# Performance work log

Measured on AMD Instinct MI355X. Metric: run time of the kernel, lower is better.

Reference implementation:

```python
import jax, jax.numpy as jnp
import numpy as np

N_NODES = 100000
N_EDGES = 1600000
IN_SIZE = 512
HID_SIZE = 256
OUT_SIZE = 16
DROP_P = 0.5


def _degrees(idx, n):
    d = jax.ops.segment_sum(jnp.ones(idx.shape[0], jnp.float32), idx, num_segments=n)
    return jnp.maximum(d, 1.0)  # DGL clamps zero degrees to 1


def graph_conv(src, dst, feat, W, b, activation=None):
    # DGL GraphConv, norm='both': D_in^{-1/2} A D_out^{-1/2} X W + b
    n = feat.shape[0]
    inv_sqrt_dout = _degrees(src, n) ** -0.5   # out-degree of source nodes
    inv_sqrt_din = _degrees(dst, n) ** -0.5    # in-degree of destination nodes
    h = feat * inv_sqrt_dout[:, None]
    h = h @ W  # in_feats >= out_feats -> transform before aggregation (same math)
    # message passing: scatter-add source messages to destinations
    h = jax.ops.segment_sum(h[src], dst, num_segments=n)
    h = h * inv_sqrt_din[:, None] + b
    if activation is not None:
        h = activation(h)
    return h


def setup_inputs() -> dict:
    key = jax.random.key(0)
    ks = jax.random.split(key, 9)
    features = jax.random.normal(ks[0], (N_NODES, IN_SIZE), jnp.float32)
    src = jax.random.randint(ks[1], (N_EDGES,), 0, N_NODES)
    dst = jax.random.randint(ks[2], (N_EDGES,), 0, N_NODES)
    W1 = jax.random.normal(ks[3], (IN_SIZE, HID_SIZE), jnp.float32) / np.sqrt(IN_SIZE).astype(np.float32)
    b1 = jnp.zeros((HID_SIZE,), jnp.float32)
    W2 = jax.random.normal(ks[4], (HID_SIZE, HID_SIZE), jnp.float32) / np.sqrt(HID_SIZE).astype(np.float32)
    b2 = jnp.zeros((HID_SIZE,), jnp.float32)
    W3 = jax.random.normal(ks[5], (HID_SIZE, OUT_SIZE), jnp.float32) / np.sqrt(HID_SIZE).astype(np.float32)
    b3 = jnp.zeros((OUT_SIZE,), jnp.float32)
    return {"features": features, "src": src, "dst": dst,
            "W1": W1, "b1": b1, "W2": W2, "b2": b2, "W3": W3, "b3": b3}


def reference(features, src, dst, W1, b1, W2, b2, W3, b3):
    # layer 0: GraphConv + relu
    h = graph_conv(src, dst, features, W1, b1, activation=jax.nn.relu)
    # dropout(0.5) before layer 1 (deterministic fixed-key mask, training semantics)
    keep = jax.random.bernoulli(jax.random.key(42), 1.0 - DROP_P, h.shape)
    h = jnp.where(keep, h / (1.0 - DROP_P), 0.0)
    # layer 1: GraphConv (no activation)
    h = graph_conv(src, dst, h, W2, b2, activation=None)
    # layer 2: plain Linear head
    return h @ W3 + b3
```

## Files before the change

### kernel.cpp

```cpp
#include <hip/hip_runtime.h>
#include <stdint.h>

#define NN    100000
#define NE    1600000
#define IN_F  512
#define HID   256
#define OUTF  16
#define NPAD  100096
#define NBK   391
#define EPB   8192

typedef unsigned int u32;
typedef __bf16 bfrag  __attribute__((ext_vector_type(8)));
typedef float  f32x4  __attribute__((ext_vector_type(4)));
typedef short  s16x8  __attribute__((ext_vector_type(8)));

__device__ __forceinline__ u32 rotl32(u32 x, int r){ return (x<<r)|(x>>(32-r)); }

__device__ __forceinline__ bool drop_keep(u32 i){
    const u32 ks0 = 0u, ks1 = 42u, ks2 = 0x1BD11BDAu ^ 0u ^ 42u;
    u32 x0 = 0u + ks0;
    u32 x1 = i  + ks1;
#define TFR(r) { x0 += x1; x1 = rotl32(x1,(r)); x1 ^= x0; }
    TFR(13) TFR(15) TFR(26) TFR(6)   x0 += ks1; x1 += ks2 + 1u;
    TFR(17) TFR(29) TFR(16) TFR(24)  x0 += ks2; x1 += ks0 + 2u;
    TFR(13) TFR(15) TFR(26) TFR(6)   x0 += ks0; x1 += ks1 + 3u;
    TFR(17) TFR(29) TFR(16) TFR(24)  x0 += ks1; x1 += ks2 + 4u;
    TFR(13) TFR(15) TFR(26) TFR(6)   x0 += ks2; x1 += ks0 + 5u;
#undef TFR
    return ((x0 ^ x1) >> 31) == 0u;
}

__device__ __forceinline__ short f2b(float f){
    union { float f; u32 u; } v; v.f = f;
    u32 r = (v.u + 0x7FFFu + ((v.u >> 16) & 1u)) >> 16;
    return (short)r;
}
__device__ __forceinline__ float blo(u32 u){ union{u32 u; float f;} v; v.u = u << 16;         return v.f; }
__device__ __forceinline__ float bhi(u32 u){ union{u32 u; float f;} v; v.u = u & 0xFFFF0000u; return v.f; }

__device__ __forceinline__ u32 cvt_pk_bf16(float lo, float hi){
    u32 r;
    asm("v_cvt_pk_bf16_f32 %0, %1, %2" : "=v"(r) : "v"(lo), "v"(hi));
    return r;
}

__device__ __forceinline__ void gll16(const void* g, void* l){
    __builtin_amdgcn_global_load_lds((const __attribute__((address_space(1))) void*)g,
                                     (__attribute__((address_space(3))) void*)l, 16, 0, 0);
}


__global__ __launch_bounds__(256) void build_hist(const int4* __restrict__ src4,
                                                  const int4* __restrict__ dst4,
                                                  int* deg_out, int* __restrict__ bcnt){
    __shared__ int h[NBK];
    int t = threadIdx.x;
    for (int i = t; i < NBK; i += 256) h[i] = 0;
    __syncthreads();
    for (int i = blockIdx.x * 256 + t; i < NE / 4; i += gridDim.x * 256) {
        int4 s = src4[i];
        int4 d = dst4[i];
        atomicAdd(&deg_out[s.x], 1);
        atomicAdd(&deg_out[s.y], 1);
        atomicAdd(&deg_out[s.z], 1);
        atomicAdd(&deg_out[s.w], 1);
        atomicAdd(&h[d.x >> 8], 1);
        atomicAdd(&h[d.y >> 8], 1);
        atomicAdd(&h[d.z >> 8], 1);
        atomicAdd(&h[d.w >> 8], 1);
    }
    __syncthreads();
    for (int i = t; i < NBK; i += 256)
        if (h[i]) atomicAdd(&bcnt[i], h[i]);
}

__global__ __launch_bounds__(256) void finalize_deg(const int* __restrict__ deg_out,
                                                    const int* __restrict__ row_ptr,
                                                    float* isdo, float* isdi){
    int i = blockIdx.x * blockDim.x + threadIdx.x;
    if (i < NN) {
        isdo[i] = rsqrtf(fmaxf((float)deg_out[i], 1.0f));
        isdi[i] = rsqrtf(fmaxf((float)(row_ptr[i + 1] - row_ptr[i]), 1.0f));
    }
}

__global__ __launch_bounds__(512) void bucket_scan(const int* __restrict__ bcnt,
                                                   int* __restrict__ bbase,
                                                   int* __restrict__ bcur,
                                                   int* __restrict__ row_ptr){
    __shared__ int sh[512];
    int t = threadIdx.x;
    int v = (t < NBK) ? bcnt[t] : 0;
    sh[t] = v;
    __syncthreads();
    for (int off = 1; off < 512; off <<= 1) {
        int a = (t >= off) ? sh[t - off] : 0;
        __syncthreads();
        sh[t] += a;
        __syncthreads();
    }
    int excl = sh[t] - v;
    if (t < NBK) { bbase[t] = excl; bcur[t] = excl; }
    if (t == 0)  { bbase[NBK] = NE; row_ptr[NN] = NE; }
}

__global__ __launch_bounds__(256) void bucket_scatter(const int* __restrict__ src,
                                                      const int* __restrict__ dst,
                                                      int* bcur, u32* __restrict__ tmp){
    __shared__ int lh[NBK];
    __shared__ int lb[NBK];
    int t = threadIdx.x;
    for (int i = t; i < NBK; i += 256) lh[i] = 0;
    __syncthreads();
    const int e0 = blockIdx.x * EPB;
    for (int k = t * 4; k < EPB; k += 1024) {
        int e = e0 + k;
        if (e < NE) {
            int4 d = *(const int4*)(dst + e);
            atomicAdd(&lh[d.x >> 8], 1);
            atomicAdd(&lh[d.y >> 8], 1);
            atomicAdd(&lh[d.z >> 8], 1);
            atomicAdd(&lh[d.w >> 8], 1);
        }
    }
    __syncthreads();
    for (int i = t; i < NBK; i += 256) {
        int c = lh[i];
        if (c) lb[i] = atomicAdd(&bcur[i], c);
        lh[i] = 0;
    }
    __syncthreads();
    for (int k = t * 4; k < EPB; k += 1024) {
        int e = e0 + k;
        if (e < NE) {
            int4 d = *(const int4*)(dst + e);
            int4 s = *(const int4*)(src + e);
            int b0 = d.x >> 8, b1 = d.y >> 8, b2 = d.z >> 8, b3 = d.w >> 8;
            int r0 = atomicAdd(&lh[b0], 1);
            tmp[lb[b0] + r0] = ((u32)s.x << 8) | ((u32)d.x & 255u);
            int r1 = atomicAdd(&lh[b1], 1);
            tmp[lb[b1] + r1] = ((u32)s.y << 8) | ((u32)d.y & 255u);
            int r2 = atomicAdd(&lh[b2], 1);
            tmp[lb[b2] + r2] = ((u32)s.z << 8) | ((u32)d.z & 255u);
            int r3 = atomicAdd(&lh[b3], 1);
            tmp[lb[b3] + r3] = ((u32)s.w << 8) | ((u32)d.w & 255u);
        }
    }
}

__global__ __launch_bounds__(256) void bucket_finalize(const u32* __restrict__ tmp,
                                                       const int* __restrict__ bbase,
                                                       int* __restrict__ row_ptr,
                                                       int* __restrict__ col_src){
    __shared__ int h[256];
    __shared__ int wtot[4];
    const int t = threadIdx.x;
    const int b = blockIdx.x;
    const int base = bbase[b];
    const int cnt  = bbase[b + 1] - base;
    h[t] = 0;
    __syncthreads();
    for (int k = t; k < cnt; k += 256)
        atomicAdd(&h[tmp[base + k] & 255u], 1);
    __syncthreads();
    int v = h[t];
    int lane = t & 63, w = t >> 6;
    int s = v;
    #pragma unroll
    for (int off = 1; off < 64; off <<= 1) {
        int u = __shfl_up(s, off);
        if (lane >= off) s += u;
    }
    if (lane == 63) wtot[w] = s;
    __syncthreads();
    int woff = 0;
    #pragma unroll
    for (int i = 0; i < 4; ++i) woff += (i < w) ? wtot[i] : 0;
    int excl = woff + s - v;
    int d = (b << 8) + t;
    if (d < NN) row_ptr[d] = base + excl;
    h[t] = excl;
    __syncthreads();
    for (int k = t; k < cnt; k += 256) {
        u32 p = tmp[base + k];
        int r = atomicAdd(&h[p & 255u], 1);
        col_src[base + r] = (int)(p >> 8);
    }
}


template<int Kd, int Nd>
__global__ __launch_bounds__(256) void convert_wt(const float* __restrict__ W,
                                                  short* __restrict__ WT){
    int i = blockIdx.x * 256 + threadIdx.x;
    if (i >= Kd * Nd) return;
    int n = i / Kd, k = i - n * Kd;
    WT[i] = f2b(W[(size_t)k * Nd + n]);
}

__global__ __launch_bounds__(256) void gemm_x(const float* __restrict__ X,
                                              const short* __restrict__ BT,
                                              const float* __restrict__ isdo,
                                              short* __restrict__ C){
    __shared__ __align__(16) float As[2 * 4096];
    __shared__ __align__(16) short Bs[2 * 4096];

    const int t = threadIdx.x;
    const int wave = t >> 6, lane = t & 63;
    const int bm = blockIdx.x * 128;
    const int bn = blockIdx.y * 128;

    const int gsw = lane ^ ((lane >> 3) & 7);
    const int rl  = gsw >> 1;
    const int pp  = gsw & 1;
    const float* pa0 = X + (size_t)(((bm + 0*32 + rl) < NN) ? (bm + 0*32 + rl) : 0) * IN_F + wave * 8 + pp * 4;
    const float* pa1 = X + (size_t)(((bm + 1*32 + rl) < NN) ? (bm + 1*32 + rl) : 0) * IN_F + wave * 8 + pp * 4;
    const float* pa2 = X + (size_t)(((bm + 2*32 + rl) < NN) ? (bm + 2*32 + rl) : 0) * IN_F + wave * 8 + pp * 4;
    const float* pa3 = X + (size_t)(((bm + 3*32 + rl) < NN) ? (bm + 3*32 + rl) : 0) * IN_F + wave * 8 + pp * 4;

    const int ch0 = wave * 128 + lane;
    const int ch1 = ch0 + 64;
    const int kb0 = ch0 >> 7, r0 = ch0 & 127;
    const int kb1 = ch1 >> 7, r1 = ch1 & 127;
    const short* pb0 = BT + (size_t)(bn + r0) * IN_F + kb0 * 8;
    const short* pb1 = BT + (size_t)(bn + r1) * IN_F + kb1 * 8;

    const int wr = (wave >> 1) * 64, wc = (wave & 1) * 64;
    const int kq = lane >> 4, r15 = lane & 15;

    f32x4 acc[4][4];
    #pragma unroll
    for (int m = 0; m < 4; ++m)
        #pragma unroll
        for (int n = 0; n < 4; ++n) acc[m][n] = (f32x4)0.0f;

#define STAGE_X(BUF, K0) { \
    float* lA = As + (BUF) * 4096 + wave * 1024; \
    gll16(pa0 + (K0), lA);       gll16(pa1 + (K0), lA + 256); \
    gll16(pa2 + (K0), lA + 512); gll16(pa3 + (K0), lA + 768); \
    short* lb = Bs + (BUF) * 4096 + (size_t)(wave * 128) * 8; \
    gll16(pb0 + (K0), lb);       gll16(pb1 + (K0), lb + 512); }

#define COMPUTE_X(BUF) { \
    const float* AsC = As + (BUF) * 4096; \
    const short* BsC = Bs + (BUF) * 4096; \
    const short* fbC = BsC + (size_t)(kq * 128 + wc + r15) * 8; \
    bfrag af[4], bfg[4]; \
    _Pragma("unroll") \
    for (int m = 0; m < 4; ++m) { \
        int r  = wr + m * 16 + r15; \
        int j  = r >> 5, rr = r & 31; \
        int g0 = 2 * rr;  int G0 = g0 ^ ((g0 >> 3) & 7); \
        int g1 = g0 + 1;  int G1 = g1 ^ ((g1 >> 3) & 7); \
        const float* base = AsC + kq * 1024 + j * 256; \
        float4 f0 = *(const float4*)(base + G0 * 4); \
        float4 f1 = *(const float4*)(base + G1 * 4); \
        uint4 q = make_uint4(cvt_pk_bf16(f0.x, f0.y), cvt_pk_bf16(f0.z, f0.w), \
                             cvt_pk_bf16(f1.x, f1.y), cvt_pk_bf16(f1.z, f1.w)); \
        af[m] = *(bfrag*)&q; \
    } \
    _Pragma("unroll") \
    for (int n = 0; n < 4; ++n) bfg[n] = *(const bfrag*)(fbC + n * 128); \
    _Pragma("unroll") \
    for (int m = 0; m < 4; ++m) \
        _Pragma("unroll") \
        for (int n = 0; n < 4; ++n) \
            acc[m][n] = __builtin_amdgcn_mfma_f32_16x16x32_bf16(af[m], bfg[n], acc[m][n], 0, 0, 0); }

    const int NT = IN_F / 32;
    STAGE_X(0, 0);
    int cur = 0;
    for (int tt = 0; tt < NT - 1; ++tt) {
        STAGE_X(cur ^ 1, (tt + 1) * 32);
        asm volatile("s_waitcnt vmcnt(6)" ::: "memory");
        __builtin_amdgcn_s_barrier();
        COMPUTE_X(cur);
        asm volatile("" ::: "memory");
        __builtin_amdgcn_s_barrier();
        cur ^= 1;
    }
    asm volatile("s_waitcnt vmcnt(0)" ::: "memory");
    __builtin_amdgcn_s_barrier();
    COMPUTE_X(cur);
#undef STAGE_X
#undef COMPUTE_X

    const int crow0 = bm + wr + (lane >> 4) * 4;
    const int ccol0 = bn + wc + (lane & 15);
    #pragma unroll
    for (int m = 0; m < 4; ++m)
        #pragma unroll
        for (int r = 0; r < 4; ++r) {
            int row = crow0 + m * 16 + r;
            float sc = (row < NN) ? isdo[row] : 0.0f;
            #pragma unroll
            for (int n = 0; n < 4; ++n)
                C[(size_t)row * HID + ccol0 + n * 16] = f2b(acc[m][n][r] * sc);
        }
}

template<int K>
__global__ __launch_bounds__(256) void gemm_bt(const short* __restrict__ A,
                                               const short* __restrict__ BT,
                                               short* __restrict__ C){
    __shared__ __align__(16) short As[2 * 4096];
    __shared__ __align__(16) short Bs[2 * 4096];

    const int t = threadIdx.x;
    const int wave = t >> 6, lane = t & 63;
    const int bm = blockIdx.x * 128;
    const int bn = blockIdx.y * 128;

    const int ch0 = wave * 128 + lane;
    const int ch1 = ch0 + 64;
    const int kb0 = ch0 >> 7, r0 = ch0 & 127;
    const int kb1 = ch1 >> 7, r1 = ch1 & 127;
    const short* pa0 = A  + (size_t)(bm + r0) * K + kb0 * 8;
    const short* pa1 = A  + (size_t)(bm + r1) * K + kb1 * 8;
    const short* pb0 = BT + (size_t)(bn + r0) * K + kb0 * 8;
    const short* pb1 = BT + (size_t)(bn + r1) * K + kb1 * 8;

    const int wr = (wave >> 1) * 64, wc = (wave & 1) * 64;
    const int frag_off = ((lane >> 4) * 128 + (lane & 15)) * 8;

    f32x4 acc[4][4];
    #pragma unroll
    for (int m = 0; m < 4; ++m)
        #pragma unroll
        for (int n = 0; n < 4; ++n) acc[m][n] = (f32x4)0.0f;

#define STAGE_B(BUF, K0) { \
    short* la = As + (BUF) * 4096 + (size_t)(wave * 128) * 8; \
    short* lb = Bs + (BUF) * 4096 + (size_t)(wave * 128) * 8; \
    gll16(pa0 + (K0), la); gll16(pa1 + (K0), la + 512); \
    gll16(pb0 + (K0), lb); gll16(pb1 + (K0), lb + 512); }

#define COMPUTE_B(BUF) { \
    const short* fa = As + (BUF) * 4096 + frag_off + wr * 8; \
    const short* fb = Bs + (BUF) * 4096 + frag_off + wc * 8; \
    bfrag af[4], bfg[4]; \
    _Pragma("unroll") \
    for (int m = 0; m < 4; ++m) af[m]  = *(const bfrag*)(fa + m * 128); \
    _Pragma("unroll") \
    for (int n = 0; n < 4; ++n) bfg[n] = *(const bfrag*)(fb + n * 128); \
    _Pragma("unroll") \
    for (int m = 0; m < 4; ++m) \
        _Pragma("unroll") \
        for (int n = 0; n < 4; ++n) \
            acc[m][n] = __builtin_amdgcn_mfma_f32_16x16x32_bf16(af[m], bfg[n], acc[m][n], 0, 0, 0); }

    const int NT = K / 32;
    STAGE_B(0, 0);
    int cur = 0;
    for (int tt = 0; tt < NT - 1; ++tt) {
        STAGE_B(cur ^ 1, (tt + 1) * 32);
        asm volatile("s_waitcnt vmcnt(4)" ::: "memory");
        __builtin_amdgcn_s_barrier();
        COMPUTE_B(cur);
        asm volatile("" ::: "memory");
        __builtin_amdgcn_s_barrier();
        cur ^= 1;
    }
    asm volatile("s_waitcnt vmcnt(0)" ::: "memory");
    __builtin_amdgcn_s_barrier();
    COMPUTE_B(cur);
#undef STAGE_B
#undef COMPUTE_B

    const int crow0 = bm + wr + (lane >> 4) * 4;
    const int ccol0 = bn + wc + (lane & 15);
    #pragma unroll
    for (int m = 0; m < 4; ++m)
        #pragma unroll
        for (int n = 0; n < 4; ++n)
            #pragma unroll
            for (int r = 0; r < 4; ++r)
                C[(size_t)(crow0 + m * 16 + r) * HID + ccol0 + n * 16] = f2b(acc[m][n][r]);
}

template<int MODE>
__global__ __launch_bounds__(256) void gather_agg(const short* __restrict__ H,
                                                  const int* __restrict__ rp,
                                                  const int* __restrict__ cs,
                                                  const float* __restrict__ isdi,
                                                  const float* __restrict__ isdo,
                                                  const float* __restrict__ bias,
                                                  short* __restrict__ out){
    const int lane = threadIdx.x & 63;
    const int node = __builtin_amdgcn_readfirstlane((int)(blockIdx.x * 4) + (int)(threadIdx.x >> 6));
    const int e0  = rp[node];
    const int end = rp[node + 1];
    const int sub = lane & 31, half = lane >> 5;
    const u32 off16 = (u32)sub * 16u;
    const char* Hb = (const char*)H;

    float a[8] = {0,0,0,0,0,0,0,0};
    float b[8] = {0,0,0,0,0,0,0,0};

#define LD4(s) (*(const uint4*)(Hb + ((((u32)(s)) << 9) | off16)))
#define ACC(A, u) { A[0]+=blo(u.x); A[1]+=bhi(u.x); A[2]+=blo(u.y); A[3]+=bhi(u.y); \
                    A[4]+=blo(u.z); A[5]+=bhi(u.z); A[6]+=blo(u.w); A[7]+=bhi(u.w); }

    int eb = e0;
    for (; eb + 16 <= end; eb += 16) {
        int t0 = cs[eb+0],  t1 = cs[eb+1],  t2 = cs[eb+2],  t3 = cs[eb+3];
        int t4 = cs[eb+4],  t5 = cs[eb+5],  t6 = cs[eb+6],  t7 = cs[eb+7];
        int t8 = cs[eb+8],  t9 = cs[eb+9],  tA = cs[eb+10], tB = cs[eb+11];
        int tC = cs[eb+12], tD = cs[eb+13], tE = cs[eb+14], tF = cs[eb+15];
        int s0 = half ? t1 : t0;
        int s1 = half ? t3 : t2;
        int s2 = half ? t5 : t4;
        int s3 = half ? t7 : t6;
        int s4 = half ? t9 : t8;
        int s5 = half ? tB : tA;
        int s6 = half ? tD : tC;
        int s7 = half ? tF : tE;
        uint4 u0 = LD4(s0), u1 = LD4(s1), u2 = LD4(s2), u3 = LD4(s3);
        uint4 u4 = LD4(s4), u5 = LD4(s5), u6 = LD4(s6), u7 = LD4(s7);
        ACC(a, u0); ACC(b, u1); ACC(a, u2); ACC(b, u3);
        ACC(a, u4); ACC(b, u5); ACC(a, u6); ACC(b, u7);
    }
    for (; eb + 8 <= end; eb += 8) {
        int t0 = cs[eb+0], t1 = cs[eb+1], t2 = cs[eb+2], t3 = cs[eb+3];
        int t4 = cs[eb+4], t5 = cs[eb+5], t6 = cs[eb+6], t7 = cs[eb+7];
        int s0 = half ? t1 : t0;
        int s1 = half ? t3 : t2;
        int s2 = half ? t5 : t4;
        int s3 = half ? t7 : t6;
        uint4 u0 = LD4(s0), u1 = LD4(s1), u2 = LD4(s2), u3 = LD4(s3);
        ACC(a, u0); ACC(b, u1); ACC(a, u2); ACC(b, u3);
    }
    for (; eb + 2 <= end; eb += 2) {
        int t0 = cs[eb], t1 = cs[eb+1];
        int s = half ? t1 : t0;
        uint4 u = LD4(s);
        ACC(a, u);
    }
    if (eb < end) {
        int s = cs[eb];
        uint4 u = LD4(s);
        if (half == 0) { ACC(a, u); }
    }
#undef ACC
#undef LD4
    #pragma unroll
    for (int j = 0; j < 8; ++j) a[j] += b[j];

    const int srcl = lane >> 1;
    const bool oddq = (lane & 1) != 0;
    float v[4];
    #pragma unroll
    for (int j = 0; j < 4; ++j) {
        float p0 = __shfl(a[j],     srcl);
        float p1 = __shfl(a[j + 4], srcl);
        float q0 = __shfl(a[j],     srcl + 32);
        float q1 = __shfl(a[j + 4], srcl + 32);
        v[j] = oddq ? (p1 + q1) : (p0 + q0);
    }

    float sd = isdi[node];
    float4 bb = *(const float4*)(bias + lane * 4);
    float h0 = v[0] * sd + bb.x;
    float h1 = v[1] * sd + bb.y;
    float h2 = v[2] * sd + bb.z;
    float h3 = v[3] * sd + bb.w;

    if (MODE == 0) {
        float so2 = 2.0f * isdo[node];
        u32 base = (u32)node * HID + (u32)lane * 4;
        h0 = drop_keep(base + 0) ? fmaxf(h0, 0.f) * so2 : 0.f;
        h1 = drop_keep(base + 1) ? fmaxf(h1, 0.f) * so2 : 0.f;
        h2 = drop_keep(base + 2) ? fmaxf(h2, 0.f) * so2 : 0.f;
        h3 = drop_keep(base + 3) ? fmaxf(h3, 0.f) * so2 : 0.f;
    }

    uint2 wv;
    wv.x = ((u32)(unsigned short)f2b(h1) << 16) | (u32)(unsigned short)f2b(h0);
    wv.y = ((u32)(unsigned short)f2b(h3) << 16) | (u32)(unsigned short)f2b(h2);
    *(uint2*)((char*)out + (size_t)node * 512 + (u32)lane * 8u) = wv;
}

__global__ __launch_bounds__(256) void head_kernel(const short* __restrict__ H2,
                                                   const float* __restrict__ W3,
                                                   const float* __restrict__ b3,
                                                   float* __restrict__ out){
    __shared__ float W3s[HID * OUTF];
    __shared__ short rows[16][HID + 8];
    int t = threadIdx.x;
    for (int i = t; i < HID * OUTF; i += 256) W3s[i] = W3[i];
    const int n0 = blockIdx.x * 16;
    for (int c = t; c < 16 * 32; c += 256) {
        int r = c >> 5, cc = c & 31;
        *(s16x8*)(&rows[r][cc * 8]) = *(const s16x8*)(H2 + (size_t)(n0 + r) * HID + cc * 8);
    }
    __syncthreads();
    int nl = t >> 4, k = t & 15;
    float acc = 0.0f;
    #pragma unroll 4
    for (int j = 0; j < HID; ++j)
        acc += blo((u32)(unsigned short)rows[nl][j]) * W3s[j * OUTF + k];
    out[(size_t)(n0 + nl) * OUTF + k] = acc + b3[k];
}

extern "C" void kernel_launch(void* const* d_in, const int* in_sizes, int n_in,
                              void* d_out, int out_size, void* d_ws, size_t ws_size,
                              hipStream_t stream) {
    const float* X   = (const float*)d_in[0];
    const int*   src = (const int*)  d_in[1];
    const int*   dst = (const int*)  d_in[2];
    const float* W1  = (const float*)d_in[3];
    const float* b1  = (const float*)d_in[4];
    const float* W2  = (const float*)d_in[5];
    const float* b2  = (const float*)d_in[6];
    const float* W3  = (const float*)d_in[7];
    const float* b3  = (const float*)d_in[8];
    float* out = (float*)d_out;

    char* ws = (char*)d_ws;
    size_t o = 0;
    int*   deg_out = (int*)  (ws + o); o += (size_t)NN * 4;
    int*   bcnt    = (int*)  (ws + o); o += (size_t)NBK * 4;
    float* isdo    = (float*)(ws + o); o += (size_t)NN * 4;
    float* isdi    = (float*)(ws + o); o += (size_t)NN * 4;
    int*   row_ptr = (int*)  (ws + o); o += (size_t)(NN + 1) * 4;
    int*   bbase   = (int*)  (ws + o); o += (size_t)(NBK + 1) * 4;
    int*   bcur    = (int*)  (ws + o); o += (size_t)NBK * 4;
    int*   col_src = (int*)  (ws + o); o += (size_t)NE * 4;
    o = (o + 255) & ~(size_t)255;
    short* W1t = (short*)(ws + o); o += (size_t)IN_F * HID * 2;
    short* W2t = (short*)(ws + o); o += (size_t)HID * HID * 2;
    o = (o + 255) & ~(size_t)255;
    short* hA    = (short*)(ws + o); o += (size_t)NPAD * HID * 2;
    short* hB    = (short*)(ws + o); o += (size_t)NPAD * HID * 2;
    short* h2pre = (short*)(ws + o); o += (size_t)NPAD * HID * 2;
    if (ws_size < o) return;
    short* h2  = hA;
    u32*   tmp = (u32*)hB;

    const size_t zlen = (size_t)NN * 4 + (size_t)NBK * 4;
    hipMemsetAsync(deg_out, 0, zlen, stream);

    build_hist<<<256, 256, 0, stream>>>((const int4*)src, (const int4*)dst, deg_out, bcnt);
    bucket_scan<<<1, 512, 0, stream>>>(bcnt, bbase, bcur, row_ptr);
    bucket_scatter<<<(NE + EPB - 1) / EPB, 256, 0, stream>>>(src, dst, bcur, tmp);
    bucket_finalize<<<NBK, 256, 0, stream>>>(tmp, bbase, row_ptr, col_src);
    finalize_deg<<<(NN + 255) / 256, 256, 0, stream>>>(deg_out, row_ptr, isdo, isdi);

    convert_wt<IN_F, HID><<<IN_F * HID / 256, 256, 0, stream>>>(W1, W1t);
    convert_wt<HID, HID><<<HID * HID / 256, 256, 0, stream>>>(W2, W2t);

    dim3 ggrid(NPAD / 128, 2);

    gemm_x<<<ggrid, 256, 0, stream>>>(X, W1t, isdo, hA);
    gather_agg<0><<<NN / 4, 256, 0, stream>>>(hA, row_ptr, col_src, isdi, isdo, b1, hB);

    gemm_bt<HID><<<ggrid, 256, 0, stream>>>(hB, W2t, h2pre);
    gather_agg<1><<<NN / 4, 256, 0, stream>>>(h2pre, row_ptr, col_src, isdi, isdo, b2, h2);

    head_kernel<<<NN / 16, 256, 0, stream>>>(h2, W3, b3, out);
}
```

Measured before the change: 538.3 us.

## Widen GEMM tiles to full 256-column output so A is loaded once

Both dense GEMMs (feature×W1 and hidden×W2) now use a 128×256 block tile covering the whole hidden dimension, replacing the 2-wide grid in N. Each A tile, including the large fp32 input feature matrix, is read from global memory once instead of twice. In exchange each wave holds twice as many accumulators and the shared-memory B buffer doubles, which raises register pressure and may reduce occupancy. The block count also halves, to about 782.

```diff
diff --git a/kernel.cpp b/kernel.cpp
--- a/kernel.cpp
+++ b/kernel.cpp
@@ -204,12 +204,11 @@
                                               const float* __restrict__ isdo,
                                               short* __restrict__ C){
     __shared__ __align__(16) float As[2 * 4096];
-    __shared__ __align__(16) short Bs[2 * 4096];
+    __shared__ __align__(16) short Bs[2 * 8192];
 
     const int t = threadIdx.x;
     const int wave = t >> 6, lane = t & 63;
     const int bm = blockIdx.x * 128;
-    const int bn = blockIdx.y * 128;
 
     const int gsw = lane ^ ((lane >> 3) & 7);
     const int rl  = gsw >> 1;
@@ -219,34 +218,33 @@
     const float* pa2 = X + (size_t)(((bm + 2*32 + rl) < NN) ? (bm + 2*32 + rl) : 0) * IN_F + wave * 8 + pp * 4;
     const float* pa3 = X + (size_t)(((bm + 3*32 + rl) < NN) ? (bm + 3*32 + rl) : 0) * IN_F + wave * 8 + pp * 4;
 
-    const int ch0 = wave * 128 + lane;
-    const int ch1 = ch0 + 64;
-    const int kb0 = ch0 >> 7, r0 = ch0 & 127;
-    const int kb1 = ch1 >> 7, r1 = ch1 & 127;
-    const short* pb0 = BT + (size_t)(bn + r0) * IN_F + kb0 * 8;
-    const short* pb1 = BT + (size_t)(bn + r1) * IN_F + kb1 * 8;
-
-    const int wr = (wave >> 1) * 64, wc = (wave & 1) * 64;
+    const short* pb0 = BT + (size_t)(  0 + lane) * IN_F + wave * 8;
+    const short* pb1 = BT + (size_t)( 64 + lane) * IN_F + wave * 8;
+    const short* pb2 = BT + (size_t)(128 + lane) * IN_F + wave * 8;
+    const short* pb3 = BT + (size_t)(192 + lane) * IN_F + wave * 8;
+
+    const int wr = (wave >> 1) * 64;
+    const int wc = (wave & 1) * 128;
     const int kq = lane >> 4, r15 = lane & 15;
 
-    f32x4 acc[4][4];
+    f32x4 acc[4][8];
     #pragma unroll
     for (int m = 0; m < 4; ++m)
         #pragma unroll
-        for (int n = 0; n < 4; ++n) acc[m][n] = (f32x4)0.0f;
+        for (int n = 0; n < 8; ++n) acc[m][n] = (f32x4)0.0f;
 
 #define STAGE_X(BUF, K0) { \
     float* lA = As + (BUF) * 4096 + wave * 1024; \
     gll16(pa0 + (K0), lA);       gll16(pa1 + (K0), lA + 256); \
     gll16(pa2 + (K0), lA + 512); gll16(pa3 + (K0), lA + 768); \
-    short* lb = Bs + (BUF) * 4096 + (size_t)(wave * 128) * 8; \
-    gll16(pb0 + (K0), lb);       gll16(pb1 + (K0), lb + 512); }
+    short* lB = Bs + (BUF) * 8192 + wave * 2048; \
+    gll16(pb0 + (K0), lB);        gll16(pb1 + (K0), lB + 512); \
+    gll16(pb2 + (K0), lB + 1024); gll16(pb3 + (K0), lB + 1536); }
 
 #define COMPUTE_X(BUF) { \
     const float* AsC = As + (BUF) * 4096; \
-    const short* BsC = Bs + (BUF) * 4096; \
-    const short* fbC = BsC + (size_t)(kq * 128 + wc + r15) * 8; \
-    bfrag af[4], bfg[4]; \
+    const short* BsC = Bs + (BUF) * 8192; \
+    bfrag af[4], bfg[8]; \
     _Pragma("unroll") \
     for (int m = 0; m < 4; ++m) { \
         int r  = wr + m * 16 + r15; \
@@ -261,11 +259,12 @@
         af[m] = *(bfrag*)&q; \
     } \
     _Pragma("unroll") \
-    for (int n = 0; n < 4; ++n) bfg[n] = *(const bfrag*)(fbC + n * 128); \
+    for (int n = 0; n < 8; ++n) \
+        bfg[n] = *(const bfrag*)(BsC + (size_t)(kq * 256 + wc + n * 16 + r15) * 8); \
     _Pragma("unroll") \
     for (int m = 0; m < 4; ++m) \
         _Pragma("unroll") \
-        for (int n = 0; n < 4; ++n) \
+        for (int n = 0; n < 8; ++n) \
             acc[m][n] = __builtin_amdgcn_mfma_f32_16x16x32_bf16(af[m], bfg[n], acc[m][n], 0, 0, 0); }
 
     const int NT = IN_F / 32;
@@ -273,7 +272,7 @@
     int cur = 0;
     for (int tt = 0; tt < NT - 1; ++tt) {
         STAGE_X(cur ^ 1, (tt + 1) * 32);
-        asm volatile("s_waitcnt vmcnt(6)" ::: "memory");
+        asm volatile("s_waitcnt vmcnt(8)" ::: "memory");
         __builtin_amdgcn_s_barrier();
         COMPUTE_X(cur);
         asm volatile("" ::: "memory");
@@ -287,7 +286,7 @@
 #undef COMPUTE_X
 
     const int crow0 = bm + wr + (lane >> 4) * 4;
-    const int ccol0 = bn + wc + (lane & 15);
+    const int ccol0 = wc + r15;
     #pragma unroll
     for (int m = 0; m < 4; ++m)
         #pragma unroll
@@ -295,7 +294,7 @@
             int row = crow0 + m * 16 + r;
             float sc = (row < NN) ? isdo[row] : 0.0f;
             #pragma unroll
-            for (int n = 0; n < 4; ++n)
+            for (int n = 0; n < 8; ++n)
                 C[(size_t)row * HID + ccol0 + n * 16] = f2b(acc[m][n][r] * sc);
         }
 }
@@ -305,49 +304,50 @@
                                                const short* __restrict__ BT,
                                                short* __restrict__ C){
     __shared__ __align__(16) short As[2 * 4096];
-    __shared__ __align__(16) short Bs[2 * 4096];
+    __shared__ __align__(16) short Bs[2 * 8192];
 
     const int t = threadIdx.x;
     const int wave = t >> 6, lane = t & 63;
     const int bm = blockIdx.x * 128;
-    const int bn = blockIdx.y * 128;
-
-    const int ch0 = wave * 128 + lane;
-    const int ch1 = ch0 + 64;
-    const int kb0 = ch0 >> 7, r0 = ch0 & 127;
-    const int kb1 = ch1 >> 7, r1 = ch1 & 127;
-    const short* pa0 = A  + (size_t)(bm + r0) * K + kb0 * 8;
-    const short* pa1 = A  + (size_t)(bm + r1) * K + kb1 * 8;
-    const short* pb0 = BT + (size_t)(bn + r0) * K + kb0 * 8;
-    const short* pb1 = BT + (size_t)(bn + r1) * K + kb1 * 8;
-
-    const int wr = (wave >> 1) * 64, wc = (wave & 1) * 64;
-    const int frag_off = ((lane >> 4) * 128 + (lane & 15)) * 8;
-
-    f32x4 acc[4][4];
+
+    const short* pa0 = A + (size_t)(bm + lane)      * K + wave * 8;
+    const short* pa1 = A + (size_t)(bm + 64 + lane) * K + wave * 8;
+    const short* pb0 = BT + (size_t)(  0 + lane) * K + wave * 8;
+    const short* pb1 = BT + (size_t)( 64 + lane) * K + wave * 8;
+    const short* pb2 = BT + (size_t)(128 + lane) * K + wave * 8;
+    const short* pb3 = BT + (size_t)(192 + lane) * K + wave * 8;
+
+    const int wr = (wave >> 1) * 64;
+    const int wc = (wave & 1) * 128;
+    const int kq = lane >> 4, r15 = lane & 15;
+
+    f32x4 acc[4][8];
     #pragma unroll
     for (int m = 0; m < 4; ++m)
         #pragma unroll
-        for (int n = 0; n < 4; ++n) acc[m][n] = (f32x4)0.0f;
+        for (int n = 0; n < 8; ++n) acc[m][n] = (f32x4)0.0f;
 
 #define STAGE_B(BUF, K0) { \
-    short* la = As + (BUF) * 4096 + (size_t)(wave * 128) * 8; \
-    short* lb = Bs + (BUF) * 4096 + (size_t)(wave * 128) * 8; \
-    gll16(pa0 + (K0), la); gll16(pa1 + (K0), la + 512); \
-    gll16(pb0 + (K0), lb); gll16(pb1 + (K0), lb + 512); }
+    short* lA = As + (BUF) * 4096 + wave * 1024; \
+    gll16(pa0 + (K0), lA); gll16(pa1 + (K0), lA + 512); \
+    short* lB = Bs + (BUF) * 8192 + wave * 2048; \
+    gll16(pb0 + (K0), lB);        gll16(pb1 + (K0), lB + 512); \
+    gll16(pb2 + (K0), lB + 1024); gll16(pb3 + (K0), lB + 1536); }
 
 #define COMPUTE_B(BUF) { \
-    const short* fa = As + (BUF) * 4096 + frag_off + wr * 8; \
-    const short* fb = Bs + (BUF) * 4096 + frag_off + wc * 8; \
-    bfrag af[4], bfg[4]; \
+    const short* AsC = As + (BUF) * 4096; \
+    const short* BsC = Bs + (BUF) * 8192; \
+    bfrag af[4], bfg[8]; \
     _Pragma("unroll") \
-    for (int m = 0; m < 4; ++m) af[m]  = *(const bfrag*)(fa + m * 128); \
+    for (int m = 0; m < 4; ++m) \
+        af[m] = *(const bfrag*)(AsC + (size_t)(kq * 128 + wr + m * 16 + r15) * 8); \
     _Pragma("unroll") \
-    for (int n = 0; n < 4; ++n) bfg[n] = *(const bfrag*)(fb + n * 128); \
+    for (int n = 0; n < 8; ++n) \
+        bfg[n] = *(const bfrag*)(BsC + (size_t)(kq * 256 + wc + n * 16 + r15) * 8); \
     _Pragma("unroll") \
     for (int m = 0; m < 4; ++m) \
         _Pragma("unroll") \
-        for (int n = 0; n < 4; ++n) \
+        for (int n = 0; n < 8; ++n) \
             acc[m][n] = __builtin_amdgcn_mfma_f32_16x16x32_bf16(af[m], bfg[n], acc[m][n], 0, 0, 0); }
 
     const int NT = K / 32;
@@ -355,7 +355,7 @@
     int cur = 0;
     for (int tt = 0; tt < NT - 1; ++tt) {
         STAGE_B(cur ^ 1, (tt + 1) * 32);
-        asm volatile("s_waitcnt vmcnt(4)" ::: "memory");
+        asm volatile("s_waitcnt vmcnt(6)" ::: "memory");
         __builtin_amdgcn_s_barrier();
         COMPUTE_B(cur);
         asm volatile("" ::: "memory");
@@ -369,11 +369,11 @@
 #undef COMPUTE_B
 
     const int crow0 = bm + wr + (lane >> 4) * 4;
-    const int ccol0 = bn + wc + (lane & 15);
+    const int ccol0 = wc + r15;
     #pragma unroll
     for (int m = 0; m < 4; ++m)
         #pragma unroll
-        for (int n = 0; n < 4; ++n)
+        for (int n = 0; n < 8; ++n)
             #pragma unroll
             for (int r = 0; r < 4; ++r)
                 C[(size_t)(crow0 + m * 16 + r) * HID + ccol0 + n * 16] = f2b(acc[m][n][r]);
@@ -550,12 +550,10 @@
     convert_wt<IN_F, HID><<<IN_F * HID / 256, 256, 0, stream>>>(W1, W1t);
     convert_wt<HID, HID><<<HID * HID / 256, 256, 0, stream>>>(W2, W2t);
 
-    dim3 ggrid(NPAD / 128, 2);
-
-    gemm_x<<<ggrid, 256, 0, stream>>>(X, W1t, isdo, hA);
+    gemm_x<<<NPAD / 128, 256, 0, stream>>>(X, W1t, isdo, hA);
     gather_agg<0><<<NN / 4, 256, 0, stream>>>(hA, row_ptr, col_src, isdi, isdo, b1, hB);
 
-    gemm_bt<HID><<<ggrid, 256, 0, stream>>>(hB, W2t, h2pre);
+    gemm_bt<HID><<<NPAD / 128, 256, 0, stream>>>(hB, W2t, h2pre);
     gather_agg<1><<<NN / 4, 256, 0, stream>>>(h2pre, row_ptr, col_src, isdi, isdo, b2, h2);
 
     head_kernel<<<NN / 16, 256, 0, stream>>>(h2, W3, b3, out);
```

New measurement: 511.2 us. -5.0%, faster.
